# Kernel optimization log

Hardware: AMD Instinct MI355X
Metric: run time of the kernel (lower is better)

Reference implementation:

```python
import jax, jax.numpy as jnp
import numpy as np

N, E = 50000, 800000
IN_C, HID, OUT_C = 100, 128, 40
LAYERS, GROUPS, CODES = 3, 3, 16
BETA = 0.98
EPS = 1e-5


def setup_inputs() -> dict:
    key = jax.random.key(0)
    ks = jax.random.split(key, 16)
    lin = lambda k, i, o: (jax.random.normal(k, (i, o), jnp.float32) / np.sqrt(i)).astype(jnp.float32)
    d = {}
    d["x"] = jax.random.normal(ks[0], (N, IN_C), jnp.float32)
    d["src"] = jax.random.randint(ks[1], (E,), 0, N, jnp.int32)
    d["dst"] = jax.random.randint(ks[2], (E,), 0, N, jnp.int32)
    # SAGEConv params: lin_l (aggregated, with bias) and lin_r (root, no bias)
    d["W0a"], d["W0r"], d["b0"] = lin(ks[3], IN_C, HID), lin(ks[4], IN_C, HID), jnp.zeros((HID,), jnp.float32)
    d["W1a"], d["W1r"], d["b1"] = lin(ks[5], HID, HID), lin(ks[6], HID, HID), jnp.zeros((HID,), jnp.float32)
    d["W2a"], d["W2r"], d["b2"] = lin(ks[7], HID, HID), lin(ks[8], HID, HID), jnp.zeros((HID,), jnp.float32)
    # BatchNorm (eval mode: running stats) for first num_layers-1 = 2 layers
    d["bn_gamma"] = jnp.ones((2, HID), jnp.float32)
    d["bn_beta"] = jnp.zeros((2, HID), jnp.float32)
    d["bn_mean"] = jnp.zeros((2, HID), jnp.float32)
    d["bn_var"] = jnp.ones((2, HID), jnp.float32)
    # Residual VQ codebooks: [layer, group, num_codes, feature]
    d["codebooks"] = 0.1 * jax.random.normal(ks[9], (LAYERS, GROUPS, CODES, HID), jnp.float32)
    d["lin_W"] = lin(ks[10], HID, OUT_C)
    d["lin_b"] = jnp.zeros((OUT_C,), jnp.float32)
    return d


def _sage_conv(h, src, dst, Wa, Wr, b):
    # mean neighbor aggregation (PyG SAGEConv, aggr='mean')
    msg = h[src]                                              # [E, d]
    agg = jax.ops.segment_sum(msg, dst, num_segments=N)       # [N, d]
    deg = jax.ops.segment_sum(jnp.ones((E,), h.dtype), dst, num_segments=N)
    agg = agg / jnp.maximum(deg, 1.0)[:, None]
    return agg @ Wa + b + h @ Wr


def _rvq(h, cb):
    # residual vector quantization over GROUPS codebooks; cb: [G, K, D]
    res, quant, ids = h, jnp.zeros_like(h), []
    for g in range(GROUPS):
        c = cb[g]                                             # [K, D]
        d2 = (jnp.sum(res * res, -1, keepdims=True)
              - 2.0 * res @ c.T + jnp.sum(c * c, -1))          # [N, K]
        idx = jnp.argmin(d2, axis=-1)
        q = c[idx]
        quant = quant + q
        res = res - q
        ids.append(idx)
    sg = jax.lax.stop_gradient
    loss = (BETA * jnp.mean((h - sg(quant)) ** 2)
            + (1.0 - BETA) * jnp.mean((sg(h) - quant) ** 2))
    return loss, jnp.stack(ids, axis=1)                        # [N, G] int


def reference(x, src, dst, W0a, W0r, b0, W1a, W1r, b1, W2a, W2r, b2,
              bn_gamma, bn_beta, bn_mean, bn_var, codebooks, lin_W, lin_b):
    Ws = [(W0a, W0r, b0), (W1a, W1r, b1), (W2a, W2r, b2)]
    h = x
    total_loss = jnp.float32(0.0)
    id_list = []
    for i in range(LAYERS - 1):
        h = _sage_conv(h, src, dst, *Ws[i])
        h = (h - bn_mean[i]) * jax.lax.rsqrt(bn_var[i] + EPS) * bn_gamma[i] + bn_beta[i]
        h = jax.nn.relu(h)                                     # dropout: eval mode (identity)
        loss, ids = _rvq(h, codebooks[i])
        total_loss = total_loss + loss
        id_list.append(ids)
    h = _sage_conv(h, src, dst, *Ws[-1])
    loss, ids = _rvq(h, codebooks[-1])
    total_loss = total_loss + loss
    id_list.append(ids)
    out = h @ lin_W + lin_b
    return out, total_loss, jnp.concatenate(id_list, axis=1)
```

## Files before the change

kernel.cpp:

```cpp
#include <hip/hip_runtime.h>

#define NN 50000
#define HID 128
#define IN_C 100
#define OUT_C 40

__global__ __launch_bounds__(256)
void hist_kernel(const int* __restrict__ dst, int* __restrict__ deg, int E) {
    int e = blockIdx.x * 256 + threadIdx.x;
    if (e < E) atomicAdd(&deg[dst[e]], 1);
}

__global__ __launch_bounds__(1024)
void scan_kernel(const int* __restrict__ deg, int* __restrict__ row_start,
                 int* __restrict__ cursor, int N) {
    __shared__ int s[1024];
    const int t = threadIdx.x;
    int running = 0;
    for (int c0 = 0; c0 < N; c0 += 1024) {
        int i = c0 + t;
        int v = (i < N) ? deg[i] : 0;
        s[t] = v;
        __syncthreads();
        for (int off = 1; off < 1024; off <<= 1) {
            int x = (t >= off) ? s[t - off] : 0;
            __syncthreads();
            s[t] += x;
            __syncthreads();
        }
        if (i < N) {
            int ex = running + s[t] - v;
            row_start[i] = ex;
            cursor[i] = ex;
        }
        running += s[1023];
        __syncthreads();
    }
    if (t == 0) row_start[N] = running;
}

__global__ __launch_bounds__(256)
void scatter_kernel(const int* __restrict__ src, const int* __restrict__ dst,
                    int* __restrict__ cursor, int* __restrict__ csr_src, int E) {
    int e = blockIdx.x * 256 + threadIdx.x;
    if (e < E) {
        int pos = atomicAdd(&cursor[dst[e]], 1);
        csr_src[pos] = src[e];
    }
}

template<int K, bool HAS_BN, typename TIN>
__global__ __launch_bounds__(256, 4)
void transform_fused(const TIN* __restrict__ h_in,
                     const int* __restrict__ row_start, const int* __restrict__ csr_src,
                     const float* __restrict__ Wa, const float* __restrict__ Wr,
                     const float* __restrict__ b,
                     const float* __restrict__ gamma, const float* __restrict__ beta,
                     const float* __restrict__ mean, const float* __restrict__ var,
                     double* __restrict__ h_out) {
    __shared__ double s_agg[4][K];
    __shared__ double s_h[4][K];
    const int t = threadIdx.x;
    const int w = t >> 6;
    const int lane = t & 63;
    const int n0 = blockIdx.x * 4;

    {
        const int n = n0 + w;
        const int r0 = row_start[n], r1 = row_start[n + 1];
        const int f0 = lane, f1 = lane + 64;
        double a0 = 0.0, a1 = 0.0, c0 = 0.0, c1 = 0.0;
        int i = r0;
        for (; i + 1 < r1; i += 2) {
            const int s0 = csr_src[i], s1 = csr_src[i + 1];
            const TIN* p0 = h_in + (size_t)s0 * K;
            const TIN* p1 = h_in + (size_t)s1 * K;
            if (f0 < K) { a0 += (double)p0[f0]; c0 += (double)p1[f0]; }
            if (f1 < K) { a1 += (double)p0[f1]; c1 += (double)p1[f1]; }
        }
        if (i < r1) {
            const int s0 = csr_src[i];
            const TIN* p0 = h_in + (size_t)s0 * K;
            if (f0 < K) a0 += (double)p0[f0];
            if (f1 < K) a1 += (double)p0[f1];
        }
        const int deg = r1 - r0;
        const double dd = (double)(deg > 1 ? deg : 1);
        const TIN* pr = h_in + (size_t)n * K;
        if (f0 < K) { s_agg[w][f0] = (a0 + c0) / dd; s_h[w][f0] = (double)pr[f0]; }
        if (f1 < K) { s_agg[w][f1] = (a1 + c1) / dd; s_h[w][f1] = (double)pr[f1]; }
    }
    __syncthreads();

    const int col = t & 127;
    const int pr2 = t >> 7;
    double accA = (double)b[col];
    double accB = accA;
#pragma unroll 4
    for (int k = 0; k < K; ++k) {
        const double wa = (double)Wa[(size_t)k * HID + col];
        const double wr = (double)Wr[(size_t)k * HID + col];
        accA += s_agg[pr2][k] * wa + s_h[pr2][k] * wr;
        accB += s_agg[pr2 + 2][k] * wa + s_h[pr2 + 2][k] * wr;
    }

    double scale = 1.0, shift = 0.0;
    if (HAS_BN) {
        scale = (double)gamma[col] / sqrt((double)var[col] + 1e-5);
        shift = (double)beta[col] - (double)mean[col] * scale;
    }
    double vA = accA, vB = accB;
    if (HAS_BN) {
        vA = vA * scale + shift; vA = vA > 0.0 ? vA : 0.0;
        vB = vB * scale + shift; vB = vB > 0.0 ? vB : 0.0;
    }
    h_out[(size_t)(n0 + pr2) * HID + col] = vA;
    h_out[(size_t)(n0 + pr2 + 2) * HID + col] = vB;
}

__global__ __launch_bounds__(256)
void rvq_kernel(const double* __restrict__ h, const float* __restrict__ cb,
                float* __restrict__ ids_out, int id_col0,
                double* __restrict__ loss_part) {
    constexpr int NPB = 16;
    __shared__ float s_cb[3 * 16 * 129];
    __shared__ float s_cc32[3][16];
    __shared__ double s_res[4][128];
    __shared__ double s_ws[4];
    const int t = threadIdx.x;
    const int w = t >> 6, lane = t & 63;

    for (int idx = t; idx < 3 * 16 * 128; idx += 256) {
        int kk = idx >> 7, j = idx & 127;
        s_cb[kk * 129 + j] = cb[idx];
    }
    __syncthreads();
    if (t < 48) {
        const float* c = &s_cb[t * 129];
        double s = 0.0;
        for (int j = 0; j < 128; j++) { double cj = (double)c[j]; s += cj * cj; }
        s_cc32[t >> 4][t & 15] = (float)s;
    }
    __syncthreads();

    double wave_loss = 0.0;
    const int n0 = blockIdx.x * NPB;
    const int k = lane & 15, q = lane >> 4;

    for (int it = 0; it < NPB / 4; ++it) {
        const int n = n0 + it * 4 + w;
        s_res[w][lane] = h[(size_t)n * 128 + lane];
        s_res[w][lane + 64] = h[(size_t)n * 128 + lane + 64];
        __syncthreads();

        for (int g = 0; g < 3; ++g) {
            double r0 = s_res[w][lane], r1 = s_res[w][lane + 64];
            double pr = r0 * r0 + r1 * r1;
            pr += __shfl_xor(pr, 1, 64);
            pr += __shfl_xor(pr, 2, 64);
            pr += __shfl_xor(pr, 4, 64);
            pr += __shfl_xor(pr, 8, 64);
            pr += __shfl_xor(pr, 16, 64);
            pr += __shfl_xor(pr, 32, 64);
            const float rr32 = (float)pr;

            const float* c = &s_cb[(g * 16 + k) * 129];
            double dot = 0.0;
#pragma unroll
            for (int j2 = 0; j2 < 32; ++j2) {
                int j = q * 32 + ((j2 + q * 8) & 31);
                dot += s_res[w][j] * (double)c[j];
            }
            dot += __shfl_xor(dot, 16, 64);
            dot += __shfl_xor(dot, 32, 64);

            const float rc32 = (float)dot;
            const float t1 = rr32 - 2.0f * rc32;
            const float d2 = t1 + s_cc32[g][k];

            float bv = d2; int bk = k;
            {
                float ov; int ok;
                ov = __shfl_xor(bv, 1, 64); ok = __shfl_xor(bk, 1, 64);
                if (ov < bv || (ov == bv && ok < bk)) { bv = ov; bk = ok; }
                ov = __shfl_xor(bv, 2, 64); ok = __shfl_xor(bk, 2, 64);
                if (ov < bv || (ov == bv && ok < bk)) { bv = ov; bk = ok; }
                ov = __shfl_xor(bv, 4, 64); ok = __shfl_xor(bk, 4, 64);
                if (ov < bv || (ov == bv && ok < bk)) { bv = ov; bk = ok; }
                ov = __shfl_xor(bv, 8, 64); ok = __shfl_xor(bk, 8, 64);
                if (ov < bv || (ov == bv && ok < bk)) { bv = ov; bk = ok; }
            }
            if (lane == 0)
                ids_out[(size_t)n * 9 + id_col0 + g] = (float)bk;

            __syncthreads();
            s_res[w][lane]      -= (double)s_cb[(g * 16 + bk) * 129 + lane];
            s_res[w][lane + 64] -= (double)s_cb[(g * 16 + bk) * 129 + lane + 64];
            __syncthreads();
        }
        double r0 = s_res[w][lane], r1 = s_res[w][lane + 64];
        wave_loss += r0 * r0 + r1 * r1;
        __syncthreads();
    }

    wave_loss += __shfl_xor(wave_loss, 1, 64);
    wave_loss += __shfl_xor(wave_loss, 2, 64);
    wave_loss += __shfl_xor(wave_loss, 4, 64);
    wave_loss += __shfl_xor(wave_loss, 8, 64);
    wave_loss += __shfl_xor(wave_loss, 16, 64);
    wave_loss += __shfl_xor(wave_loss, 32, 64);
    if (lane == 0) s_ws[w] = wave_loss;
    __syncthreads();
    if (t == 0) loss_part[blockIdx.x] = s_ws[0] + s_ws[1] + s_ws[2] + s_ws[3];
}

__global__ __launch_bounds__(128)
void linear_kernel(const double* __restrict__ h, const float* __restrict__ W,
                   const float* __restrict__ b, float* __restrict__ out, int N) {
    constexpr int NODES = 32;
    __shared__ float s_w[HID * OUT_C];
    __shared__ float s_b[OUT_C];
    __shared__ double s_h[HID];
    const int t = threadIdx.x;
    for (int idx = t; idx < HID * OUT_C; idx += 128) s_w[idx] = W[idx];
    if (t < OUT_C) s_b[t] = b[t];
    __syncthreads();
    const int n0 = blockIdx.x * NODES;
    for (int ni = 0; ni < NODES; ++ni) {
        int n = n0 + ni;
        if (n >= N) break;
        s_h[t] = h[(size_t)n * HID + t];
        __syncthreads();
        if (t < OUT_C) {
            double acc = (double)s_b[t];
            for (int kk = 0; kk < HID; kk++)
                acc += s_h[kk] * (double)s_w[kk * OUT_C + t];
            out[(size_t)n * OUT_C + t] = (float)acc;
        }
        __syncthreads();
    }
}

__global__ __launch_bounds__(256)
void finalize_kernel(const double* __restrict__ loss_part, int M,
                     float* __restrict__ out_loss) {
    __shared__ double s[256];
    const int t = threadIdx.x;
    double v = 0.0;
    for (int i = t; i < M; i += 256) v += loss_part[i];
    s[t] = v;
    __syncthreads();
    for (int off = 128; off; off >>= 1) {
        if (t < off) s[t] += s[t + off];
        __syncthreads();
    }
    if (t == 0) out_loss[0] = (float)(s[0] / ((double)NN * (double)HID));
}

extern "C" void kernel_launch(void* const* d_in, const int* in_sizes, int n_in,
                              void* d_out, int out_size, void* d_ws, size_t ws_size,
                              hipStream_t stream) {
    const float* x    = (const float*)d_in[0];
    const int*   src  = (const int*)d_in[1];
    const int*   dst  = (const int*)d_in[2];
    const float* W0a = (const float*)d_in[3];
    const float* W0r = (const float*)d_in[4];
    const float* b0  = (const float*)d_in[5];
    const float* W1a = (const float*)d_in[6];
    const float* W1r = (const float*)d_in[7];
    const float* b1  = (const float*)d_in[8];
    const float* W2a = (const float*)d_in[9];
    const float* W2r = (const float*)d_in[10];
    const float* b2  = (const float*)d_in[11];
    const float* bn_gamma = (const float*)d_in[12];
    const float* bn_beta  = (const float*)d_in[13];
    const float* bn_mean  = (const float*)d_in[14];
    const float* bn_var   = (const float*)d_in[15];
    const float* cb    = (const float*)d_in[16];
    const float* lin_W = (const float*)d_in[17];
    const float* lin_b = (const float*)d_in[18];

    const int E = in_sizes[1];

    float* out      = (float*)d_out;
    float* out_loss = out + (size_t)NN * OUT_C;
    float* out_ids  = out_loss + 1;

    char* base = (char*)d_ws;
    int* deg_i     = (int*)base;
    int* row_start = deg_i + NN;
    int* cursor    = row_start + NN + 1;
    int* csr_src   = cursor + NN;
    size_t int_bytes = ((size_t)(3 * NN + 1 + E) * 4 + 255) & ~(size_t)255;
    double* loss_part = (double*)(base + int_bytes);
    double* h1 = loss_part + 3 * 3125 + 7;
    double* h2 = h1 + (size_t)NN * HID;

    const int cb_layer = 3 * 16 * HID;
    const int NB_RVQ = NN / 16;

    hipMemsetAsync(deg_i, 0, NN * sizeof(int), stream);
    hist_kernel<<<(E + 255) / 256, 256, 0, stream>>>(dst, deg_i, E);
    scan_kernel<<<1, 1024, 0, stream>>>(deg_i, row_start, cursor, NN);
    scatter_kernel<<<(E + 255) / 256, 256, 0, stream>>>(src, dst, cursor, csr_src, E);

    transform_fused<IN_C, true, float><<<NN / 4, 256, 0, stream>>>(
        x, row_start, csr_src, W0a, W0r, b0, bn_gamma, bn_beta, bn_mean, bn_var, h1);
    rvq_kernel<<<NB_RVQ, 256, 0, stream>>>(h1, cb + 0 * cb_layer, out_ids, 0, loss_part);

    transform_fused<HID, true, double><<<NN / 4, 256, 0, stream>>>(
        h1, row_start, csr_src, W1a, W1r, b1,
        bn_gamma + HID, bn_beta + HID, bn_mean + HID, bn_var + HID, h2);
    rvq_kernel<<<NB_RVQ, 256, 0, stream>>>(h2, cb + 1 * cb_layer, out_ids, 3, loss_part + NB_RVQ);

    transform_fused<HID, false, double><<<NN / 4, 256, 0, stream>>>(
        h2, row_start, csr_src, W2a, W2r, b2, nullptr, nullptr, nullptr, nullptr, h1);
    rvq_kernel<<<NB_RVQ, 256, 0, stream>>>(h1, cb + 2 * cb_layer, out_ids, 6, loss_part + 2 * NB_RVQ);

    linear_kernel<<<(NN + 31) / 32, 128, 0, stream>>>(h1, lin_W, lin_b, out, NN);
    finalize_kernel<<<1, 256, 0, stream>>>(loss_part, 3 * NB_RVQ, out_loss);
}
```

Measured before the change: 1.122 ms.

## Fuse RVQ into SAGE layer kernel and parallelize degree scan

Merges each layer's aggregation/transform kernel with its residual-VQ kernel, so the quantizer works on the freshly computed row held in shared memory instead of re-reading it from global memory. Blocks grow to 512 threads covering 8 nodes, and each lane now gathers two adjacent features. The single-block serial scan that builds row offsets is replaced by a three-kernel multi-block scan. In exchange, every block reloads the codebook and shared memory per block rises, which may limit occupancy. The launch count also goes up for the scan stage.

Measured after the change: 1.029 ms. 8.3% less time.

```diff
diff --git a/kernel.cpp b/kernel.cpp
--- a/kernel.cpp
+++ b/kernel.cpp
@@ -11,32 +11,54 @@
     if (e < E) atomicAdd(&deg[dst[e]], 1);
 }
 
-__global__ __launch_bounds__(1024)
-void scan_kernel(const int* __restrict__ deg, int* __restrict__ row_start,
-                 int* __restrict__ cursor, int N) {
-    __shared__ int s[1024];
-    const int t = threadIdx.x;
-    int running = 0;
-    for (int c0 = 0; c0 < N; c0 += 1024) {
-        int i = c0 + t;
-        int v = (i < N) ? deg[i] : 0;
-        s[t] = v;
-        __syncthreads();
-        for (int off = 1; off < 1024; off <<= 1) {
-            int x = (t >= off) ? s[t - off] : 0;
-            __syncthreads();
-            s[t] += x;
-            __syncthreads();
-        }
-        if (i < N) {
-            int ex = running + s[t] - v;
-            row_start[i] = ex;
-            cursor[i] = ex;
-        }
-        running += s[1023];
-        __syncthreads();
-    }
-    if (t == 0) row_start[N] = running;
+__global__ __launch_bounds__(256)
+void chunk_sum_kernel(const int* __restrict__ deg, int* __restrict__ chunk_sums, int N) {
+    __shared__ int s[256];
+    const int t = threadIdx.x;
+    const int i = blockIdx.x * 256 + t;
+    s[t] = (i < N) ? deg[i] : 0;
+    __syncthreads();
+    for (int o = 128; o; o >>= 1) { if (t < o) s[t] += s[t + o]; __syncthreads(); }
+    if (t == 0) chunk_sums[blockIdx.x] = s[0];
+}
+
+__global__ __launch_bounds__(256)
+void chunk_scan_kernel(int* __restrict__ chunk_sums, int M) {
+    __shared__ int s[256];
+    const int t = threadIdx.x;
+    int v = (t < M) ? chunk_sums[t] : 0;
+    s[t] = v;
+    __syncthreads();
+    for (int o = 1; o < 256; o <<= 1) {
+        int x = (t >= o) ? s[t - o] : 0;
+        __syncthreads();
+        s[t] += x;
+        __syncthreads();
+    }
+    if (t < M) chunk_sums[t] = s[t] - v;
+}
+
+__global__ __launch_bounds__(256)
+void chunk_apply_kernel(const int* __restrict__ deg, const int* __restrict__ chunk_sums,
+                        int* __restrict__ row_start, int* __restrict__ cursor, int N) {
+    __shared__ int s[256];
+    const int t = threadIdx.x;
+    const int i = blockIdx.x * 256 + t;
+    int v = (i < N) ? deg[i] : 0;
+    s[t] = v;
+    __syncthreads();
+    for (int o = 1; o < 256; o <<= 1) {
+        int x = (t >= o) ? s[t - o] : 0;
+        __syncthreads();
+        s[t] += x;
+        __syncthreads();
+    }
+    if (i < N) {
+        int ex = chunk_sums[blockIdx.x] + s[t] - v;
+        row_start[i] = ex;
+        cursor[i] = ex;
+        if (i == N - 1) row_start[N] = ex + v;
+    }
 }
 
 __global__ __launch_bounds__(256)
@@ -50,91 +72,86 @@
 }
 
 template<int K, bool HAS_BN, typename TIN>
-__global__ __launch_bounds__(256, 4)
-void transform_fused(const TIN* __restrict__ h_in,
-                     const int* __restrict__ row_start, const int* __restrict__ csr_src,
-                     const float* __restrict__ Wa, const float* __restrict__ Wr,
-                     const float* __restrict__ b,
-                     const float* __restrict__ gamma, const float* __restrict__ beta,
-                     const float* __restrict__ mean, const float* __restrict__ var,
-                     double* __restrict__ h_out) {
-    __shared__ double s_agg[4][K];
-    __shared__ double s_h[4][K];
-    const int t = threadIdx.x;
-    const int w = t >> 6;
-    const int lane = t & 63;
-    const int n0 = blockIdx.x * 4;
+__global__ __launch_bounds__(512, 6)
+void layer_fused(const TIN* __restrict__ h_in,
+                 const int* __restrict__ row_start, const int* __restrict__ csr_src,
+                 const float* __restrict__ Wa, const float* __restrict__ Wr,
+                 const float* __restrict__ b,
+                 const float* __restrict__ gamma, const float* __restrict__ beta,
+                 const float* __restrict__ mean, const float* __restrict__ var,
+                 const float* __restrict__ cb,
+                 double* __restrict__ h_out,
+                 float* __restrict__ ids_out, int id_col0,
+                 double* __restrict__ loss_part) {
+    __shared__ double s_agg[8][HID];
+    __shared__ double s_h[8][HID];
+    __shared__ float s_cb[3 * 16 * 129];
+    __shared__ float s_cc32[3][16];
+    __shared__ double s_ws[8];
+    const int t = threadIdx.x;
+    const int w = t >> 6, lane = t & 63;
+    const int n0 = blockIdx.x * 8;
 
     {
         const int n = n0 + w;
         const int r0 = row_start[n], r1 = row_start[n + 1];
-        const int f0 = lane, f1 = lane + 64;
-        double a0 = 0.0, a1 = 0.0, c0 = 0.0, c1 = 0.0;
-        int i = r0;
-        for (; i + 1 < r1; i += 2) {
-            const int s0 = csr_src[i], s1 = csr_src[i + 1];
-            const TIN* p0 = h_in + (size_t)s0 * K;
-            const TIN* p1 = h_in + (size_t)s1 * K;
-            if (f0 < K) { a0 += (double)p0[f0]; c0 += (double)p1[f0]; }
-            if (f1 < K) { a1 += (double)p0[f1]; c1 += (double)p1[f1]; }
-        }
-        if (i < r1) {
-            const int s0 = csr_src[i];
-            const TIN* p0 = h_in + (size_t)s0 * K;
-            if (f0 < K) a0 += (double)p0[f0];
-            if (f1 < K) a1 += (double)p0[f1];
-        }
-        const int deg = r1 - r0;
-        const double dd = (double)(deg > 1 ? deg : 1);
-        const TIN* pr = h_in + (size_t)n * K;
-        if (f0 < K) { s_agg[w][f0] = (a0 + c0) / dd; s_h[w][f0] = (double)pr[f0]; }
-        if (f1 < K) { s_agg[w][f1] = (a1 + c1) / dd; s_h[w][f1] = (double)pr[f1]; }
-    }
-    __syncthreads();
+        const int f0 = 2 * lane;
+        if (f0 < K) {
+            double a0 = 0.0, a1 = 0.0, c0 = 0.0, c1 = 0.0;
+            int i = r0;
+            for (; i + 1 < r1; i += 2) {
+                const TIN* p0 = h_in + (size_t)csr_src[i] * K + f0;
+                const TIN* p1 = h_in + (size_t)csr_src[i + 1] * K + f0;
+                a0 += (double)p0[0]; a1 += (double)p0[1];
+                c0 += (double)p1[0]; c1 += (double)p1[1];
+            }
+            if (i < r1) {
+                const TIN* p0 = h_in + (size_t)csr_src[i] * K + f0;
+                a0 += (double)p0[0]; a1 += (double)p0[1];
+            }
+            const int deg = r1 - r0;
+            const double dd = (double)(deg > 1 ? deg : 1);
+            const TIN* pr = h_in + (size_t)n * K + f0;
+            s_agg[w][f0]     = (a0 + c0) / dd;
+            s_agg[w][f0 + 1] = (a1 + c1) / dd;
+            s_h[w][f0]     = (double)pr[0];
+            s_h[w][f0 + 1] = (double)pr[1];
+        }
+    }
+    __syncthreads();
+
+    for (int idx = t; idx < 3 * 16 * 128; idx += 512)
+        s_cb[(idx >> 7) * 129 + (idx & 127)] = cb[idx];
 
     const int col = t & 127;
-    const int pr2 = t >> 7;
+    const int p4 = t >> 7;
     double accA = (double)b[col];
     double accB = accA;
 #pragma unroll 4
     for (int k = 0; k < K; ++k) {
         const double wa = (double)Wa[(size_t)k * HID + col];
         const double wr = (double)Wr[(size_t)k * HID + col];
-        accA += s_agg[pr2][k] * wa + s_h[pr2][k] * wr;
-        accB += s_agg[pr2 + 2][k] * wa + s_h[pr2 + 2][k] * wr;
-    }
-
-    double scale = 1.0, shift = 0.0;
-    if (HAS_BN) {
-        scale = (double)gamma[col] / sqrt((double)var[col] + 1e-5);
-        shift = (double)beta[col] - (double)mean[col] * scale;
-    }
-    double vA = accA, vB = accB;
-    if (HAS_BN) {
-        vA = vA * scale + shift; vA = vA > 0.0 ? vA : 0.0;
-        vB = vB * scale + shift; vB = vB > 0.0 ? vB : 0.0;
-    }
-    h_out[(size_t)(n0 + pr2) * HID + col] = vA;
-    h_out[(size_t)(n0 + pr2 + 2) * HID + col] = vB;
-}
-
-__global__ __launch_bounds__(256)
-void rvq_kernel(const double* __restrict__ h, const float* __restrict__ cb,
-                float* __restrict__ ids_out, int id_col0,
-                double* __restrict__ loss_part) {
-    constexpr int NPB = 16;
-    __shared__ float s_cb[3 * 16 * 129];
-    __shared__ float s_cc32[3][16];
-    __shared__ double s_res[4][128];
-    __shared__ double s_ws[4];
-    const int t = threadIdx.x;
-    const int w = t >> 6, lane = t & 63;
-
-    for (int idx = t; idx < 3 * 16 * 128; idx += 256) {
-        int kk = idx >> 7, j = idx & 127;
-        s_cb[kk * 129 + j] = cb[idx];
-    }
-    __syncthreads();
+        accA += s_agg[p4][k] * wa + s_h[p4][k] * wr;
+        accB += s_agg[p4 + 4][k] * wa + s_h[p4 + 4][k] * wr;
+    }
+    __syncthreads();
+
+    {
+        double scale = 1.0, shift = 0.0;
+        if (HAS_BN) {
+            scale = (double)gamma[col] / sqrt((double)var[col] + 1e-5);
+            shift = (double)beta[col] - (double)mean[col] * scale;
+        }
+        double vA = accA, vB = accB;
+        if (HAS_BN) {
+            vA = vA * scale + shift; vA = vA > 0.0 ? vA : 0.0;
+            vB = vB * scale + shift; vB = vB > 0.0 ? vB : 0.0;
+        }
+        h_out[(size_t)(n0 + p4) * HID + col] = vA;
+        h_out[(size_t)(n0 + p4 + 4) * HID + col] = vB;
+        s_agg[p4][col] = vA;
+        s_agg[p4 + 4][col] = vB;
+    }
     if (t < 48) {
         const float* c = &s_cb[t * 129];
         double s = 0.0;
@@ -143,18 +160,13 @@
     }
     __syncthreads();
 
-    double wave_loss = 0.0;
-    const int n0 = blockIdx.x * NPB;
-    const int k = lane & 15, q = lane >> 4;
-
-    for (int it = 0; it < NPB / 4; ++it) {
-        const int n = n0 + it * 4 + w;
-        s_res[w][lane] = h[(size_t)n * 128 + lane];
-        s_res[w][lane + 64] = h[(size_t)n * 128 + lane + 64];
-        __syncthreads();
+    {
+        double* res = &s_agg[w][0];
+        const int n = n0 + w;
+        const int k = lane & 15, q = lane >> 4;
 
         for (int g = 0; g < 3; ++g) {
-            double r0 = s_res[w][lane], r1 = s_res[w][lane + 64];
+            double r0 = res[lane], r1 = res[lane + 64];
             double pr = r0 * r0 + r1 * r1;
             pr += __shfl_xor(pr, 1, 64);
             pr += __shfl_xor(pr, 2, 64);
@@ -169,7 +181,7 @@
 #pragma unroll
             for (int j2 = 0; j2 < 32; ++j2) {
                 int j = q * 32 + ((j2 + q * 8) & 31);
-                dot += s_res[w][j] * (double)c[j];
+                dot += res[j] * (double)c[j];
             }
             dot += __shfl_xor(dot, 16, 64);
             dot += __shfl_xor(dot, 32, 64);
@@ -193,25 +205,26 @@
             if (lane == 0)
                 ids_out[(size_t)n * 9 + id_col0 + g] = (float)bk;
 
-            __syncthreads();
-            s_res[w][lane]      -= (double)s_cb[(g * 16 + bk) * 129 + lane];
-            s_res[w][lane + 64] -= (double)s_cb[(g * 16 + bk) * 129 + lane + 64];
-            __syncthreads();
-        }
-        double r0 = s_res[w][lane], r1 = s_res[w][lane + 64];
-        wave_loss += r0 * r0 + r1 * r1;
-        __syncthreads();
-    }
-
-    wave_loss += __shfl_xor(wave_loss, 1, 64);
-    wave_loss += __shfl_xor(wave_loss, 2, 64);
-    wave_loss += __shfl_xor(wave_loss, 4, 64);
-    wave_loss += __shfl_xor(wave_loss, 8, 64);
-    wave_loss += __shfl_xor(wave_loss, 16, 64);
-    wave_loss += __shfl_xor(wave_loss, 32, 64);
-    if (lane == 0) s_ws[w] = wave_loss;
-    __syncthreads();
-    if (t == 0) loss_part[blockIdx.x] = s_ws[0] + s_ws[1] + s_ws[2] + s_ws[3];
+            res[lane]      -= (double)s_cb[(g * 16 + bk) * 129 + lane];
+            res[lane + 64] -= (double)s_cb[(g * 16 + bk) * 129 + lane + 64];
+        }
+        double r0 = res[lane], r1 = res[lane + 64];
+        double wl = r0 * r0 + r1 * r1;
+        wl += __shfl_xor(wl, 1, 64);
+        wl += __shfl_xor(wl, 2, 64);
+        wl += __shfl_xor(wl, 4, 64);
+        wl += __shfl_xor(wl, 8, 64);
+        wl += __shfl_xor(wl, 16, 64);
+        wl += __shfl_xor(wl, 32, 64);
+        if (lane == 0) s_ws[w] = wl;
+    }
+    __syncthreads();
+    if (t == 0) {
+        double s = 0.0;
+#pragma unroll
+        for (int i = 0; i < 8; i++) s += s_ws[i];
+        loss_part[blockIdx.x] = s;
+    }
 }
 
 __global__ __launch_bounds__(128)
@@ -287,36 +300,40 @@
     float* out_ids  = out_loss + 1;
 
     char* base = (char*)d_ws;
-    int* deg_i     = (int*)base;
-    int* row_start = deg_i + NN;
-    int* cursor    = row_start + NN + 1;
-    int* csr_src   = cursor + NN;
-    size_t int_bytes = ((size_t)(3 * NN + 1 + E) * 4 + 255) & ~(size_t)255;
+    int* deg_i      = (int*)base;
+    int* row_start  = deg_i + NN;
+    int* cursor     = row_start + NN + 1;
+    int* csr_src    = cursor + NN;
+    int* chunk_sums = csr_src + E;
+    size_t int_bytes = ((size_t)(3 * NN + 1 + E + 256) * 4 + 255) & ~(size_t)255;
     double* loss_part = (double*)(base + int_bytes);
-    double* h1 = loss_part + 3 * 3125 + 7;
+    double* h1 = loss_part + 3 * 6250 + 6;
     double* h2 = h1 + (size_t)NN * HID;
 
     const int cb_layer = 3 * 16 * HID;
-    const int NB_RVQ = NN / 16;
+    const int NB = NN / 8;
+    const int NCHUNK = (NN + 255) / 256;
 
     hipMemsetAsync(deg_i, 0, NN * sizeof(int), stream);
     hist_kernel<<<(E + 255) / 256, 256, 0, stream>>>(dst, deg_i, E);
-    scan_kernel<<<1, 1024, 0, stream>>>(deg_i, row_start, cursor, NN);
+    chunk_sum_kernel<<<NCHUNK, 256, 0, stream>>>(deg_i, chunk_sums, NN);
+    chunk_scan_kernel<<<1, 256, 0, stream>>>(chunk_sums, NCHUNK);
+    chunk_apply_kernel<<<NCHUNK, 256, 0, stream>>>(deg_i, chunk_sums, row_start, cursor, NN);
     scatter_kernel<<<(E + 255) / 256, 256, 0, stream>>>(src, dst, cursor, csr_src, E);
 
-    transform_fused<IN_C, true, float><<<NN / 4, 256, 0, stream>>>(
-        x, row_start, csr_src, W0a, W0r, b0, bn_gamma, bn_beta, bn_mean, bn_var, h1);
-    rvq_kernel<<<NB_RVQ, 256, 0, stream>>>(h1, cb + 0 * cb_layer, out_ids, 0, loss_part);
-
-    transform_fused<HID, true, double><<<NN / 4, 256, 0, stream>>>(
+    layer_fused<IN_C, true, float><<<NB, 512, 0, stream>>>(
+        x, row_start, csr_src, W0a, W0r, b0, bn_gamma, bn_beta, bn_mean, bn_var,
+        cb + 0 * cb_layer, h1, out_ids, 0, loss_part);
+
+    layer_fused<HID, true, double><<<NB, 512, 0, stream>>>(
         h1, row_start, csr_src, W1a, W1r, b1,
-        bn_gamma + HID, bn_beta + HID, bn_mean + HID, bn_var + HID, h2);
-    rvq_kernel<<<NB_RVQ, 256, 0, stream>>>(h2, cb + 1 * cb_layer, out_ids, 3, loss_part + NB_RVQ);
-
-    transform_fused<HID, false, double><<<NN / 4, 256, 0, stream>>>(
-        h2, row_start, csr_src, W2a, W2r, b2, nullptr, nullptr, nullptr, nullptr, h1);
-    rvq_kernel<<<NB_RVQ, 256, 0, stream>>>(h1, cb + 2 * cb_layer, out_ids, 6, loss_part + 2 * NB_RVQ);
+        bn_gamma + HID, bn_beta + HID, bn_mean + HID, bn_var + HID,
+        cb + 1 * cb_layer, h2, out_ids, 3, loss_part + NB);
+
+    layer_fused<HID, false, double><<<NB, 512, 0, stream>>>(
+        h2, row_start, csr_src, W2a, W2r, b2, nullptr, nullptr, nullptr, nullptr,
+        cb + 2 * cb_layer, h1, out_ids, 6, loss_part + 2 * NB);
 
     linear_kernel<<<(NN + 31) / 32, 128, 0, stream>>>(h1, lin_W, lin_b, out, NN);
-    finalize_kernel<<<1, 256, 0, stream>>>(loss_part, 3 * NB_RVQ, out_loss);
-}
+    finalize_kernel<<<1, 256, 0, stream>>>(loss_part, 3 * NB, out_loss);
+}
```
